# Kernel optimization log

Measured on AMD Instinct MI355X. Metric: run time of the kernel, lower is better.

The kernel has to match this reference:

```python
import jax, jax.numpy as jnp
import numpy as np

PRECISION = 127.0

def _pwb_quantize(t):
    # Pulse-width binary mapping: clip to [-1, 1] (layer constraint) and
    # quantize to `precision` discrete levels, as PWBMapper realizes weights.
    t = jnp.clip(t, -1.0, 1.0)
    return jnp.round(t * PRECISION) / PRECISION

def setup_inputs() -> dict:
    key = jax.random.key(0)
    k1, k2, k3 = jax.random.split(key, 3)
    B, DIN, DOUT = 4096, 2048, 2048
    x = jax.random.normal(k1, (B, DIN), dtype=jnp.float32)
    # tf.random_normal_initializer default stddev = 0.05
    W = jax.random.normal(k2, (DIN, DOUT), dtype=jnp.float32) * 0.05
    b = jax.random.normal(k3, (DOUT,), dtype=jnp.float32) * 0.05
    return {"x": x, "W": W, "b": b}

def reference(x, W, b):
    # Fused equivalent of the per-sample / per-neuron Python loops:
    # each neuron's PWB step is a dot product with the quantized weight
    # column; the bias neuron adds the quantized bias. Then activation.
    Wq = _pwb_quantize(W)            # [DIN, DOUT]
    bq = _pwb_quantize(b)            # [DOUT]
    y = jnp.einsum('bi,io->bo', x, Wq) + bq
    return jax.nn.relu(y)
```

## Files before the change

kernel.cpp:

```cpp
#include <hip/hip_runtime.h>
#include <hip/hip_bf16.h>
#include <stdint.h>


typedef __attribute__((ext_vector_type(4))) int i32x4;

#define BM 128
#define BN 64
#define BK 64

__device__ __forceinline__ float pwb_clip(float w) {
    return fminf(fmaxf(w, -1.f), 1.f);
}

__device__ __forceinline__ void gl16(const int8_t* g, int8_t* l) {
    __builtin_amdgcn_global_load_lds(
        (const __attribute__((address_space(1))) void*)(g),
        (__attribute__((address_space(3))) void*)(l),
        16, 0, 0);
}

#define WAIT_VM4   asm volatile("s_waitcnt vmcnt(4)" ::: "memory");
#define WAIT_VM2   asm volatile("s_waitcnt vmcnt(2)" ::: "memory");
#define WAIT_VM0   asm volatile("s_waitcnt vmcnt(0)" ::: "memory");
#define BAR()      __builtin_amdgcn_s_barrier();

__global__ void pwb_prep(const float* __restrict__ x, const float* __restrict__ W,
                         int8_t* __restrict__ xq, int8_t* __restrict__ Wq,
                         float* __restrict__ scales, int DIN, int DOUT, int xblocks) {
    __shared__ __align__(16) float smem[4 * 2048];
    const int tid = threadIdx.x;
    const size_t KB = (size_t)(DIN >> 6) << 10;

    if ((int)blockIdx.x < xblocks) {
        const int wv = tid >> 6, l = tid & 63;
        const int row = blockIdx.x * 4 + wv;
        const float4* xr = (const float4*)(x + (size_t)row * DIN);
        float* xs = smem + wv * 2048;
        const int J = DIN >> 8;
        float m = 0.f;
        for (int j = 0; j < J; ++j) {
            float4 v = xr[j * 64 + l];
            *(float4*)&xs[j * 256 + l * 4] = v;
            m = fmaxf(m, fmaxf(fmaxf(fabsf(v.x), fabsf(v.y)),
                               fmaxf(fabsf(v.z), fabsf(v.w))));
        }
#pragma unroll
        for (int d = 1; d < 64; d <<= 1) m = fmaxf(m, __shfl_xor(m, d));
        const float r = (m > 0.f) ? 127.f / m : 0.f;
        if (l == 0) scales[row] = m / 16129.f;
        int8_t* orow_ = xq + (size_t)(row >> 4) * KB + (row & 15) * 64;
        for (int j = 0; j < J; ++j) {
            float4 v = *(const float4*)&xs[j * 256 + l * 4];
            int q0 = (int)rintf(v.x * r), q1 = (int)rintf(v.y * r);
            int q2 = (int)rintf(v.z * r), q3 = (int)rintf(v.w * r);
            uint32_t u = (uint32_t)(q0 & 255) | ((uint32_t)(q1 & 255) << 8) |
                         ((uint32_t)(q2 & 255) << 16) | ((uint32_t)(q3 & 255) << 24);
            *(uint32_t*)(orow_ + (size_t)(j * 4 + (l >> 4)) * 1024 + (l & 15) * 4) = u;
        }
    } else {
        int8_t* tq = (int8_t*)smem;
        const int wb = blockIdx.x - xblocks;
        const int gw = DOUT >> 6;
        const int c0 = (wb % gw) * 64;
        const int r0 = (wb / gw) * 64;
        const int kl = tid >> 4;
        const int nc = (tid & 15) * 4;
#pragma unroll
        for (int i = 0; i < 4; ++i) {
            int k = r0 + kl + i * 16;
            float4 wv = *(const float4*)&W[(size_t)k * DOUT + c0 + nc];
            tq[(nc + 0) * 72 + kl + i * 16] = (int8_t)rintf(pwb_clip(wv.x) * 127.f);
            tq[(nc + 1) * 72 + kl + i * 16] = (int8_t)rintf(pwb_clip(wv.y) * 127.f);
            tq[(nc + 2) * 72 + kl + i * 16] = (int8_t)rintf(pwb_clip(wv.z) * 127.f);
            tq[(nc + 3) * 72 + kl + i * 16] = (int8_t)rintf(pwb_clip(wv.w) * 127.f);
        }
        __syncthreads();
        const int nl = tid >> 2, cc = (tid & 3) * 16;
        uint4 u;
        u.x = *(const uint32_t*)&tq[nl * 72 + cc + 0];
        u.y = *(const uint32_t*)&tq[nl * 72 + cc + 4];
        u.z = *(const uint32_t*)&tq[nl * 72 + cc + 8];
        u.w = *(const uint32_t*)&tq[nl * 72 + cc + 12];
        const int n = c0 + nl;
        *(uint4*)(Wq + (size_t)(n >> 4) * KB +
                  (size_t)(r0 >> 6) * 1024 + (n & 15) * 64 + cc) = u;
    }
}

__global__ __launch_bounds__(256, 4) void pwb_gemmq(
    const int8_t* __restrict__ A,
    const int8_t* __restrict__ Bt,
    const float* __restrict__ scales,
    const float* __restrict__ b,
    float* __restrict__ C,
    int M, int N, int K, int GN, int nwg) {
    __shared__ __align__(16) int8_t lA[4][BM * BK];

    const int tid = threadIdx.x;
    const int w   = tid >> 6;
    const int l   = tid & 63;
    const int lr  = l & 15;
    const int lk  = l >> 4;

    const int bid = blockIdx.x;
    const int q = nwg >> 3, r = nwg & 7;
    const int xcd = bid & 7, lin = bid >> 3;
    const int wgid = (xcd < r ? xcd * (q + 1) : r * (q + 1) + (xcd - r) * q) + lin;
    const int tm = wgid / GN, tn = wgid % GN;
    const size_t brow = (size_t)tm * BM, bcol = (size_t)tn * BN;

    const int wm = (w >> 1) * 64;
    const int wn = (w & 1) * 32;

    const int KT = K >> 6;
    const size_t KB = (size_t)KT << 10;

    const int8_t* gA[2];
#pragma unroll
    for (int i = 0; i < 2; ++i) {
        int s = tid + 256 * i;
        gA[i] = A + (size_t)((brow >> 4) + (s >> 6)) * KB + (s & 63) * 16;
    }
    const int8_t* pB = Bt + (size_t)((bcol + wn) >> 4) * KB + lr * 64 + lk * 16;
    const int offA = (wm >> 4) * 1024 + lr * 64 + lk * 16;

    i32x4 acc[4][2] = {};
    i32x4 bS0[2], bS1[2], afr[4];

#define STAGE(buf, t)                                                   \
    gl16(gA[0] + (size_t)(t) * 1024, &lA[buf][tid * 16]);               \
    gl16(gA[1] + (size_t)(t) * 1024, &lA[buf][(tid + 256) * 16]);

#define LOADB(set, t)                                                   \
    _Pragma("unroll") for (int nj = 0; nj < 2; ++nj)                    \
        set[nj] = *(const i32x4*)(pB + (size_t)nj * KB + (size_t)(t) * 1024);

#define LOADA(buf)                                                      \
    _Pragma("unroll") for (int mi = 0; mi < 4; ++mi)                    \
        afr[mi] = *(const i32x4*)&lA[buf][offA + mi * 1024];

#define MFMA8(fb)                                                       \
    __builtin_amdgcn_s_setprio(1);                                      \
    _Pragma("unroll") for (int mi = 0; mi < 4; ++mi)                    \
    _Pragma("unroll") for (int nj = 0; nj < 2; ++nj)                    \
        acc[mi][nj] = __builtin_amdgcn_mfma_i32_16x16x64_i8(            \
            afr[mi], fb[nj], acc[mi][nj], 0, 0, 0);                     \
    __builtin_amdgcn_s_setprio(0);

    STAGE(0, 0)
    LOADB(bS0, 0)
    STAGE(1, 1)
    WAIT_VM2
    BAR();

    const int T = KT;
    for (int it = 0; it < (T - 2) / 2; ++it) {
        const int t0 = 2 * it;
        LOADB(bS1, t0 + 1)
        STAGE((t0 + 2) & 3, t0 + 2)
        LOADA(t0 & 3)
        WAIT_VM4
        BAR();
        MFMA8(bS0)
        LOADB(bS0, t0 + 2)
        STAGE((t0 + 3) & 3, t0 + 3)
        LOADA((t0 + 1) & 3)
        WAIT_VM4
        BAR();
        MFMA8(bS1)
    }
    LOADB(bS1, T - 1)
    LOADA((T - 2) & 3)
    WAIT_VM2
    BAR();
    MFMA8(bS0)
    WAIT_VM0
    LOADA((T - 1) & 3)
    MFMA8(bS1)

    float bias[2];
#pragma unroll
    for (int nj = 0; nj < 2; ++nj) {
        float bv = b[bcol + wn + nj * 16 + lr];
        bias[nj] = rintf(pwb_clip(bv) * 127.f) * (1.f / 127.f);
    }

    const size_t orow = brow + wm + lk * 4;
    const size_t ocol = bcol + wn + lr;
    float4 scl[4];
#pragma unroll
    for (int mi = 0; mi < 4; ++mi)
        scl[mi] = *(const float4*)&scales[orow + mi * 16];

#pragma unroll
    for (int mi = 0; mi < 4; ++mi) {
        const float s0_ = scl[mi].x, s1_ = scl[mi].y, s2_ = scl[mi].z, s3_ = scl[mi].w;
#pragma unroll
        for (int nj = 0; nj < 2; ++nj) {
            float v0 = fmaf((float)acc[mi][nj][0], s0_, bias[nj]);
            float v1 = fmaf((float)acc[mi][nj][1], s1_, bias[nj]);
            float v2 = fmaf((float)acc[mi][nj][2], s2_, bias[nj]);
            float v3 = fmaf((float)acc[mi][nj][3], s3_, bias[nj]);
            float* cp = &C[(orow + mi * 16) * N + (ocol + nj * 16)];
            cp[0 * N] = fmaxf(v0, 0.f);
            cp[1 * N] = fmaxf(v1, 0.f);
            cp[2 * N] = fmaxf(v2, 0.f);
            cp[3 * N] = fmaxf(v3, 0.f);
        }
    }
#undef STAGE
#undef LOADB
#undef LOADA
#undef MFMA8
}

__global__ void pwb_fallback(const float* __restrict__ x, const float* __restrict__ W,
                             const float* __restrict__ b, float* __restrict__ out,
                             int M, int N, int K) {
    __shared__ float sA[16][17];
    __shared__ float sB[16][17];
    int tx = threadIdx.x, ty = threadIdx.y;
    int row = blockIdx.y * 16 + ty;
    int col = blockIdx.x * 16 + tx;
    float acc = 0.f;
    for (int kt = 0; kt < K; kt += 16) {
        sA[ty][tx] = (row < M && kt + tx < K) ? x[(size_t)row * K + kt + tx] : 0.f;
        float w = (kt + ty < K && col < N) ? W[(size_t)(kt + ty) * N + col] : 0.f;
        sB[ty][tx] = rintf(pwb_clip(w) * 127.f) * (1.f / 127.f);
        __syncthreads();
#pragma unroll
        for (int kk = 0; kk < 16; ++kk) acc += sA[ty][kk] * sB[kk][tx];
        __syncthreads();
    }
    if (row < M && col < N) {
        float v = acc + rintf(pwb_clip(b[col]) * 127.f) * (1.f / 127.f);
        out[(size_t)row * N + col] = fmaxf(v, 0.f);
    }
}

extern "C" void kernel_launch(void* const* d_in, const int* in_sizes, int n_in,
                              void* d_out, int out_size, void* d_ws, size_t ws_size,
                              hipStream_t stream) {
    const float* x = (const float*)d_in[0];
    const float* W = (const float*)d_in[1];
    const float* b = (const float*)d_in[2];
    float* out = (float*)d_out;

    const int DOUT = in_sizes[2];
    const int DIN  = in_sizes[1] / DOUT;
    const int M    = in_sizes[0] / DIN;

    size_t need = (size_t)M * DIN + (size_t)DIN * DOUT + (size_t)M * 4;
    const int T = DIN / BK;
    bool fast = (M % BM == 0) && (DOUT % 64 == 0) &&
                (DIN % 256 == 0) && (DIN <= 2048) && (T >= 4) && ((T & 1) == 0) &&
                (ws_size >= need);

    if (fast) {
        int8_t* xq = (int8_t*)d_ws;
        int8_t* Wq = xq + (size_t)M * DIN;
        float* scales = (float*)(Wq + (size_t)DIN * DOUT);

        const int xblocks = M / 4;
        const int wblocks = (DIN / 64) * (DOUT / 64);
        pwb_prep<<<xblocks + wblocks, 256, 0, stream>>>(x, W, xq, Wq, scales,
                                                        DIN, DOUT, xblocks);

        const int GM = M / BM, GN = DOUT / BN, nwg = GM * GN;
        pwb_gemmq<<<nwg, 256, 0, stream>>>(xq, Wq, scales, b, out, M, DOUT, DIN, GN, nwg);
    } else {
        dim3 g((DOUT + 15) / 16, (M + 15) / 16), blk(16, 16);
        pwb_fallback<<<g, blk, 0, stream>>>(x, W, b, out, M, DOUT, DIN);
    }
}
```

Before: 43.29 us.

## Enlarge int8 GEMM tile to 128x128 with K=128 stages and swizzled LDS

The GEMM tile grows from 128x64 to 128x128, so each wave computes a 64x64 sub-tile (4x4 MFMA accumulators) and each A fragment read from LDS is reused across more N columns. The K step per pipeline stage doubles to 128, and the A buffer moves from a 4-deep to a 3-deep ring of 16KB slots. The LDS layout gains an XOR swizzle to reduce bank conflicts. In exchange, the larger accumulator and B register sets raise register pressure, launch bounds drop to 2 waves per SIMD, and the grid has half as many workgroups.

```diff
diff --git a/kernel.cpp b/kernel.cpp
--- a/kernel.cpp
+++ b/kernel.cpp
@@ -6,8 +6,7 @@
 typedef __attribute__((ext_vector_type(4))) int i32x4;
 
 #define BM 128
-#define BN 64
-#define BK 64
+#define BN 128
 
 __device__ __forceinline__ float pwb_clip(float w) {
     return fminf(fmaxf(w, -1.f), 1.f);
@@ -21,7 +20,6 @@
 }
 
 #define WAIT_VM4   asm volatile("s_waitcnt vmcnt(4)" ::: "memory");
-#define WAIT_VM2   asm volatile("s_waitcnt vmcnt(2)" ::: "memory");
 #define WAIT_VM0   asm volatile("s_waitcnt vmcnt(0)" ::: "memory");
 #define BAR()      __builtin_amdgcn_s_barrier();
 
@@ -88,14 +86,14 @@
     }
 }
 
-__global__ __launch_bounds__(256, 4) void pwb_gemmq(
+__global__ __launch_bounds__(256, 2) void pwb_gemmq(
     const int8_t* __restrict__ A,
     const int8_t* __restrict__ Bt,
     const float* __restrict__ scales,
     const float* __restrict__ b,
     float* __restrict__ C,
     int M, int N, int K, int GN, int nwg) {
-    __shared__ __align__(16) int8_t lA[4][BM * BK];
+    __shared__ __align__(16) int8_t lA[3 * BM * 128];
 
     const int tid = threadIdx.x;
     const int w   = tid >> 6;
@@ -111,77 +109,96 @@
     const size_t brow = (size_t)tm * BM, bcol = (size_t)tn * BN;
 
     const int wm = (w >> 1) * 64;
-    const int wn = (w & 1) * 32;
+    const int wn = (w & 1) * 64;
 
     const int KT = K >> 6;
+    const int E  = K >> 7;
     const size_t KB = (size_t)KT << 10;
 
-    const int8_t* gA[2];
-#pragma unroll
-    for (int i = 0; i < 2; ++i) {
-        int s = tid + 256 * i;
-        gA[i] = A + (size_t)((brow >> 4) + (s >> 6)) * KB + (s & 63) * 16;
+    const int8_t* gSt[4];
+#pragma unroll
+    for (int i = 0; i < 4; ++i) {
+        int g = 4 * i + w;
+        int gc = (l & 3) ^ ((l >> 3) & 3);
+        gSt[i] = A + (size_t)((brow >> 4) + (g >> 1)) * KB + (size_t)(g & 1) * 1024
+                   + (l >> 2) * 64 + gc * 16;
     }
     const int8_t* pB = Bt + (size_t)((bcol + wn) >> 4) * KB + lr * 64 + lk * 16;
-    const int offA = (wm >> 4) * 1024 + lr * 64 + lk * 16;
-
-    i32x4 acc[4][2] = {};
-    i32x4 bS0[2], bS1[2], afr[4];
-
-#define STAGE(buf, t)                                                   \
-    gl16(gA[0] + (size_t)(t) * 1024, &lA[buf][tid * 16]);               \
-    gl16(gA[1] + (size_t)(t) * 1024, &lA[buf][(tid + 256) * 16]);
-
-#define LOADB(set, t)                                                   \
-    _Pragma("unroll") for (int nj = 0; nj < 2; ++nj)                    \
-        set[nj] = *(const i32x4*)(pB + (size_t)nj * KB + (size_t)(t) * 1024);
-
-#define LOADA(buf)                                                      \
-    _Pragma("unroll") for (int mi = 0; mi < 4; ++mi)                    \
-        afr[mi] = *(const i32x4*)&lA[buf][offA + mi * 1024];
-
-#define MFMA8(fb)                                                       \
-    __builtin_amdgcn_s_setprio(1);                                      \
-    _Pragma("unroll") for (int mi = 0; mi < 4; ++mi)                    \
-    _Pragma("unroll") for (int nj = 0; nj < 2; ++nj)                    \
-        acc[mi][nj] = __builtin_amdgcn_mfma_i32_16x16x64_i8(            \
-            afr[mi], fb[nj], acc[mi][nj], 0, 0, 0);                     \
-    __builtin_amdgcn_s_setprio(0);
+    const int aBase = (w >> 1) * 8192 + lr * 64 + ((lk ^ ((lr >> 1) & 3)) << 4);
+
+    i32x4 acc[4][4] = {};
+    i32x4 bS0[8], bS1[8];
+
+#define STAGE(buf, e) {                                             \
+    int8_t* d_ = &lA[(buf) * 16384];                                \
+    gl16(gSt[0] + (size_t)(e) * 2048, d_ + tid * 16);               \
+    gl16(gSt[1] + (size_t)(e) * 2048, d_ + (tid + 256) * 16);       \
+    gl16(gSt[2] + (size_t)(e) * 2048, d_ + (tid + 512) * 16);       \
+    gl16(gSt[3] + (size_t)(e) * 2048, d_ + (tid + 768) * 16); }
+
+#define LOADB(SET, e)                                               \
+    _Pragma("unroll") for (int ks = 0; ks < 2; ++ks)                \
+    _Pragma("unroll") for (int nj = 0; nj < 4; ++nj)                \
+        SET[ks * 4 + nj] = *(const i32x4*)(pB + (size_t)nj * KB +   \
+                           (size_t)(2 * (e) + ks) * 1024);
+
+#define COMPUTE(cur, SET) {                                         \
+    const int8_t* ab_ = &lA[(cur) * 16384 + aBase];                 \
+    i32x4 afr[4];                                                   \
+    _Pragma("unroll") for (int mi = 0; mi < 4; ++mi)                \
+        afr[mi] = *(const i32x4*)(ab_ + mi * 2048);                 \
+    __builtin_amdgcn_s_setprio(1);                                  \
+    _Pragma("unroll") for (int mi = 0; mi < 4; ++mi)                \
+    _Pragma("unroll") for (int nj = 0; nj < 4; ++nj)                \
+        acc[mi][nj] = __builtin_amdgcn_mfma_i32_16x16x64_i8(        \
+            afr[mi], SET[nj], acc[mi][nj], 0, 0, 0);                \
+    __builtin_amdgcn_s_setprio(0);                                  \
+    _Pragma("unroll") for (int mi = 0; mi < 4; ++mi)                \
+        afr[mi] = *(const i32x4*)(ab_ + mi * 2048 + 1024);          \
+    __builtin_amdgcn_s_setprio(1);                                  \
+    _Pragma("unroll") for (int mi = 0; mi < 4; ++mi)                \
+    _Pragma("unroll") for (int nj = 0; nj < 4; ++nj)                \
+        acc[mi][nj] = __builtin_amdgcn_mfma_i32_16x16x64_i8(        \
+            afr[mi], SET[4 + nj], acc[mi][nj], 0, 0, 0);            \
+    __builtin_amdgcn_s_setprio(0); }
 
     STAGE(0, 0)
     LOADB(bS0, 0)
     STAGE(1, 1)
-    WAIT_VM2
+    WAIT_VM4
     BAR();
 
-    const int T = KT;
-    for (int it = 0; it < (T - 2) / 2; ++it) {
-        const int t0 = 2 * it;
-        LOADB(bS1, t0 + 1)
-        STAGE((t0 + 2) & 3, t0 + 2)
-        LOADA(t0 & 3)
+    int cur = 0;
+    for (int e = 0; e < E - 2; e += 2) {
+        LOADB(bS1, e + 1)
+        {
+            int nb = cur + 2; if (nb >= 3) nb -= 3;
+            STAGE(nb, e + 2)
+        }
+        COMPUTE(cur, bS0)
         WAIT_VM4
         BAR();
-        MFMA8(bS0)
-        LOADB(bS0, t0 + 2)
-        STAGE((t0 + 3) & 3, t0 + 3)
-        LOADA((t0 + 1) & 3)
+        cur = (cur == 2) ? 0 : cur + 1;
+        LOADB(bS0, e + 2)
+        {
+            int nb = cur + 2; if (nb >= 3) nb -= 3;
+            STAGE(nb, e + 3)
+        }
+        COMPUTE(cur, bS1)
         WAIT_VM4
         BAR();
-        MFMA8(bS1)
-    }
-    LOADB(bS1, T - 1)
-    LOADA((T - 2) & 3)
-    WAIT_VM2
+        cur = (cur == 2) ? 0 : cur + 1;
+    }
+    LOADB(bS1, E - 1)
+    COMPUTE(cur, bS0)
+    WAIT_VM0
     BAR();
-    MFMA8(bS0)
-    WAIT_VM0
-    LOADA((T - 1) & 3)
-    MFMA8(bS1)
-
-    float bias[2];
-#pragma unroll
-    for (int nj = 0; nj < 2; ++nj) {
+    cur = (cur == 2) ? 0 : cur + 1;
+    COMPUTE(cur, bS1)
+
+    float bias[4];
+#pragma unroll
+    for (int nj = 0; nj < 4; ++nj) {
         float bv = b[bcol + wn + nj * 16 + lr];
         bias[nj] = rintf(pwb_clip(bv) * 127.f) * (1.f / 127.f);
     }
@@ -197,7 +214,7 @@
     for (int mi = 0; mi < 4; ++mi) {
         const float s0_ = scl[mi].x, s1_ = scl[mi].y, s2_ = scl[mi].z, s3_ = scl[mi].w;
 #pragma unroll
-        for (int nj = 0; nj < 2; ++nj) {
+        for (int nj = 0; nj < 4; ++nj) {
             float v0 = fmaf((float)acc[mi][nj][0], s0_, bias[nj]);
             float v1 = fmaf((float)acc[mi][nj][1], s1_, bias[nj]);
             float v2 = fmaf((float)acc[mi][nj][2], s2_, bias[nj]);
@@ -211,8 +228,7 @@
     }
 #undef STAGE
 #undef LOADB
-#undef LOADA
-#undef MFMA8
+#undef COMPUTE
 }
 
 __global__ void pwb_fallback(const float* __restrict__ x, const float* __restrict__ W,
@@ -252,9 +268,9 @@
     const int M    = in_sizes[0] / DIN;
 
     size_t need = (size_t)M * DIN + (size_t)DIN * DOUT + (size_t)M * 4;
-    const int T = DIN / BK;
-    bool fast = (M % BM == 0) && (DOUT % 64 == 0) &&
-                (DIN % 256 == 0) && (DIN <= 2048) && (T >= 4) && ((T & 1) == 0) &&
+    const int E = DIN >> 7;
+    bool fast = (M % BM == 0) && (DOUT % BN == 0) &&
+                (DIN % 256 == 0) && (DIN <= 2048) && (E >= 2) && ((E & 1) == 0) &&
                 (ws_size >= need);
 
     if (fast) {
```

Measured after the change: 42.18 us. 1.03x faster.

## Drop LDS staging for A and enlarge int8 GEMM tile to 128x256 with register double-buffering

Applied to the files above, without the earlier changes.

The int8 MFMA GEMM no longer stages A tiles through LDS with global_load_lds and barriers. Each wave now loads its A and B fragments straight from global memory into two register sets and alternates between them. The block tile grows from 128x64 to 128x256, giving each wave a 64x128 sub-tile of 32 accumulators, and launch bounds drop to one block per SIMD group. This removes LDS traffic and barrier syncs and raises per-wave compute intensity. The costs are heavy register use, fewer workgroups (256) for the GPU's compute units, and more reliance on L2 for the reuse LDS used to provide.

```diff
diff --git a/kernel.cpp b/kernel.cpp
--- a/kernel.cpp
+++ b/kernel.cpp
@@ -6,24 +6,11 @@
 typedef __attribute__((ext_vector_type(4))) int i32x4;
 
 #define BM 128
-#define BN 64
-#define BK 64
+#define BN 256
 
 __device__ __forceinline__ float pwb_clip(float w) {
     return fminf(fmaxf(w, -1.f), 1.f);
 }
-
-__device__ __forceinline__ void gl16(const int8_t* g, int8_t* l) {
-    __builtin_amdgcn_global_load_lds(
-        (const __attribute__((address_space(1))) void*)(g),
-        (__attribute__((address_space(3))) void*)(l),
-        16, 0, 0);
-}
-
-#define WAIT_VM4   asm volatile("s_waitcnt vmcnt(4)" ::: "memory");
-#define WAIT_VM2   asm volatile("s_waitcnt vmcnt(2)" ::: "memory");
-#define WAIT_VM0   asm volatile("s_waitcnt vmcnt(0)" ::: "memory");
-#define BAR()      __builtin_amdgcn_s_barrier();
 
 __global__ void pwb_prep(const float* __restrict__ x, const float* __restrict__ W,
                          int8_t* __restrict__ xq, int8_t* __restrict__ Wq,
@@ -88,15 +75,13 @@
     }
 }
 
-__global__ __launch_bounds__(256, 4) void pwb_gemmq(
+__global__ __launch_bounds__(256, 1) void pwb_gemmq(
     const int8_t* __restrict__ A,
     const int8_t* __restrict__ Bt,
     const float* __restrict__ scales,
     const float* __restrict__ b,
     float* __restrict__ C,
     int M, int N, int K, int GN, int nwg) {
-    __shared__ __align__(16) int8_t lA[4][BM * BK];
-
     const int tid = threadIdx.x;
     const int w   = tid >> 6;
     const int l   = tid & 63;
@@ -111,77 +96,45 @@
     const size_t brow = (size_t)tm * BM, bcol = (size_t)tn * BN;
 
     const int wm = (w >> 1) * 64;
-    const int wn = (w & 1) * 32;
+    const int wn = (w & 1) * 128;
 
     const int KT = K >> 6;
     const size_t KB = (size_t)KT << 10;
 
-    const int8_t* gA[2];
-#pragma unroll
-    for (int i = 0; i < 2; ++i) {
-        int s = tid + 256 * i;
-        gA[i] = A + (size_t)((brow >> 4) + (s >> 6)) * KB + (s & 63) * 16;
-    }
+    const int8_t* pA = A  + (size_t)((brow + wm) >> 4) * KB + lr * 64 + lk * 16;
     const int8_t* pB = Bt + (size_t)((bcol + wn) >> 4) * KB + lr * 64 + lk * 16;
-    const int offA = (wm >> 4) * 1024 + lr * 64 + lk * 16;
-
-    i32x4 acc[4][2] = {};
-    i32x4 bS0[2], bS1[2], afr[4];
-
-#define STAGE(buf, t)                                                   \
-    gl16(gA[0] + (size_t)(t) * 1024, &lA[buf][tid * 16]);               \
-    gl16(gA[1] + (size_t)(t) * 1024, &lA[buf][(tid + 256) * 16]);
-
-#define LOADB(set, t)                                                   \
-    _Pragma("unroll") for (int nj = 0; nj < 2; ++nj)                    \
-        set[nj] = *(const i32x4*)(pB + (size_t)nj * KB + (size_t)(t) * 1024);
-
-#define LOADA(buf)                                                      \
+
+    i32x4 acc[4][8] = {};
+    i32x4 a0[4], b0[8], a1[4], b1[8];
+
+#define LOADSET(AS, BS, t)                                              \
     _Pragma("unroll") for (int mi = 0; mi < 4; ++mi)                    \
-        afr[mi] = *(const i32x4*)&lA[buf][offA + mi * 1024];
-
-#define MFMA8(fb)                                                       \
-    __builtin_amdgcn_s_setprio(1);                                      \
+        AS[mi] = *(const i32x4*)(pA + (size_t)mi * KB + (size_t)(t) * 1024); \
+    _Pragma("unroll") for (int nj = 0; nj < 8; ++nj)                    \
+        BS[nj] = *(const i32x4*)(pB + (size_t)nj * KB + (size_t)(t) * 1024);
+
+#define MFMA32(AS, BS)                                                  \
     _Pragma("unroll") for (int mi = 0; mi < 4; ++mi)                    \
-    _Pragma("unroll") for (int nj = 0; nj < 2; ++nj)                    \
+    _Pragma("unroll") for (int nj = 0; nj < 8; ++nj)                    \
         acc[mi][nj] = __builtin_amdgcn_mfma_i32_16x16x64_i8(            \
-            afr[mi], fb[nj], acc[mi][nj], 0, 0, 0);                     \
-    __builtin_amdgcn_s_setprio(0);
-
-    STAGE(0, 0)
-    LOADB(bS0, 0)
-    STAGE(1, 1)
-    WAIT_VM2
-    BAR();
+            AS[mi], BS[nj], acc[mi][nj], 0, 0, 0);
+
+    LOADSET(a0, b0, 0)
+    LOADSET(a1, b1, 1)
 
     const int T = KT;
-    for (int it = 0; it < (T - 2) / 2; ++it) {
-        const int t0 = 2 * it;
-        LOADB(bS1, t0 + 1)
-        STAGE((t0 + 2) & 3, t0 + 2)
-        LOADA(t0 & 3)
-        WAIT_VM4
-        BAR();
-        MFMA8(bS0)
-        LOADB(bS0, t0 + 2)
-        STAGE((t0 + 3) & 3, t0 + 3)
-        LOADA((t0 + 1) & 3)
-        WAIT_VM4
-        BAR();
-        MFMA8(bS1)
-    }
-    LOADB(bS1, T - 1)
-    LOADA((T - 2) & 3)
-    WAIT_VM2
-    BAR();
-    MFMA8(bS0)
-    WAIT_VM0
-    LOADA((T - 1) & 3)
-    MFMA8(bS1)
-
-    float bias[2];
-#pragma unroll
-    for (int nj = 0; nj < 2; ++nj) {
+    for (int t = 0; t < T - 2; t += 2) {
+        MFMA32(a0, b0)
+        LOADSET(a0, b0, t + 2)
+        MFMA32(a1, b1)
+        LOADSET(a1, b1, t + 3)
+    }
+    MFMA32(a0, b0)
+    MFMA32(a1, b1)
+
+    float bias[8];
+#pragma unroll
+    for (int nj = 0; nj < 8; ++nj) {
         float bv = b[bcol + wn + nj * 16 + lr];
         bias[nj] = rintf(pwb_clip(bv) * 127.f) * (1.f / 127.f);
     }
@@ -197,7 +150,7 @@
     for (int mi = 0; mi < 4; ++mi) {
         const float s0_ = scl[mi].x, s1_ = scl[mi].y, s2_ = scl[mi].z, s3_ = scl[mi].w;
 #pragma unroll
-        for (int nj = 0; nj < 2; ++nj) {
+        for (int nj = 0; nj < 8; ++nj) {
             float v0 = fmaf((float)acc[mi][nj][0], s0_, bias[nj]);
             float v1 = fmaf((float)acc[mi][nj][1], s1_, bias[nj]);
             float v2 = fmaf((float)acc[mi][nj][2], s2_, bias[nj]);
@@ -209,10 +162,8 @@
             cp[3 * N] = fmaxf(v3, 0.f);
         }
     }
-#undef STAGE
-#undef LOADB
-#undef LOADA
-#undef MFMA8
+#undef LOADSET
+#undef MFMA32
 }
 
 __global__ void pwb_fallback(const float* __restrict__ x, const float* __restrict__ W,
@@ -252,8 +203,8 @@
     const int M    = in_sizes[0] / DIN;
 
     size_t need = (size_t)M * DIN + (size_t)DIN * DOUT + (size_t)M * 4;
-    const int T = DIN / BK;
-    bool fast = (M % BM == 0) && (DOUT % 64 == 0) &&
+    const int T = DIN / 64;
+    bool fast = (M % BM == 0) && (M % 4 == 0) && (DOUT % BN == 0) &&
                 (DIN % 256 == 0) && (DIN <= 2048) && (T >= 4) && ((T & 1) == 0) &&
                 (ws_size >= need);
 
```

New measurement: 44.69 us. 1.03x slower.
